# Optimization experiments

Measured on AMD Instinct MI355X. Metric: run time of the kernel, lower is better.

## Reference

```python
import jax, jax.numpy as jnp
import numpy as np
import math

N_EMBED = 1024
N_HEAD = 16
BLOCK_SIZE = 2048

def setup_inputs() -> dict:
    key = jax.random.key(0)
    k1, k2, k3, k4, k5 = jax.random.split(key, 5)
    s = 0.02
    x = jax.random.normal(k1, (2, 2048, N_EMBED), dtype=jnp.float32)
    W_qkv = jax.random.normal(k2, (N_EMBED, 3 * N_EMBED), dtype=jnp.float32) * s
    b_qkv = jax.random.normal(k3, (3 * N_EMBED,), dtype=jnp.float32) * s
    W_out = jax.random.normal(k4, (N_EMBED, N_EMBED), dtype=jnp.float32) * s
    b_out = jax.random.normal(k5, (N_EMBED,), dtype=jnp.float32) * s
    return {"x": x, "W_qkv": W_qkv, "b_qkv": b_qkv, "W_out": W_out, "b_out": b_out}

def reference(x, W_qkv, b_qkv, W_out, b_out):
    b, s, d = x.shape
    hd = d // N_HEAD  # head dim
    qkv = x @ W_qkv + b_qkv                       # [b, s, 3d]
    q, k, v = jnp.split(qkv, 3, axis=-1)
    # [b, h, s, hd]
    q = q.reshape(b, s, N_HEAD, hd).transpose(0, 2, 1, 3)
    k = k.reshape(b, s, N_HEAD, hd).transpose(0, 2, 1, 3)
    v = v.reshape(b, s, N_HEAD, hd).transpose(0, 2, 1, 3)
    scale = 1.0 / math.sqrt(hd)
    sims = jnp.einsum('bhqd,bhkd->bhqk', q, k) * scale  # [b, h, s, s]
    causal = jnp.tril(jnp.ones((s, s), dtype=bool))
    sims = jnp.where(causal[None, None], sims, -jnp.inf)
    probs = jax.nn.softmax(sims, axis=-1)
    attn = jnp.einsum('bhqk,bhkd->bhqd', probs, v)       # [b, h, s, hd]
    attn = attn.transpose(0, 2, 1, 3).reshape(b, s, d)
    return attn @ W_out + b_out
```

## Files before the change

### kernel.cpp

```cpp
#include <hip/hip_runtime.h>
#include <hip/hip_bf16.h>

typedef __attribute__((ext_vector_type(8))) short short8;
typedef __attribute__((ext_vector_type(4))) short short4v;
typedef __attribute__((ext_vector_type(4))) float f32x4;
typedef __attribute__((ext_vector_type(16))) float f32x16;
typedef __attribute__((ext_vector_type(4))) unsigned int u32x4;
typedef unsigned short u16;

__device__ __forceinline__ u16 f2bf(float f) {
  __hip_bfloat16 h = __float2bfloat16(f);
  return __builtin_bit_cast(unsigned short, h);
}

__device__ __forceinline__ unsigned pack2(float lo, float hi) {
  return (unsigned)f2bf(lo) | ((unsigned)f2bf(hi) << 16);
}

__device__ __forceinline__ void gload16(const u16* g, u16* l) {
  __builtin_amdgcn_global_load_lds(
      (const __attribute__((address_space(1))) unsigned int*)g,
      (__attribute__((address_space(3))) unsigned int*)l, 16, 0, 0);
}

__global__ void cvt_x_kernel(const float* __restrict__ in, u16* __restrict__ out, int n) {
  int i = (blockIdx.x * blockDim.x + threadIdx.x) * 4;
  if (i >= n) return;
  float4 f = *(const float4*)(in + i);
  uint2 pk;
  pk.x = pack2(f.x, f.y);
  pk.y = pack2(f.z, f.w);
  *(uint2*)(out + i) = pk;
}

__global__ void tcvt_kernel(const float* __restrict__ in, u16* __restrict__ out, int N) {
  __shared__ float tile[32][33];
  int n0 = blockIdx.x * 32, k0 = blockIdx.y * 32;
  int tx = threadIdx.x, ty = threadIdx.y;
#pragma unroll
  for (int r = 0; r < 4; ++r) {
    int k = ty + r * 8;
    tile[k][tx] = in[(size_t)(k0 + k) * N + n0 + tx];
  }
  __syncthreads();
#pragma unroll
  for (int r = 0; r < 4; ++r) {
    int n = ty + r * 8;
    out[(size_t)(n0 + n) * 1024 + k0 + tx] = f2bf(tile[tx][n]);
  }
}

template <int EPI>
__global__ __launch_bounds__(256, 2) void gemm_kernel(const u16* __restrict__ A,
                                                      const u16* __restrict__ Bt,
                                                      const float* __restrict__ bias,
                                                      void* __restrict__ outp) {
  __shared__ u16 Al[128 * 64];
  __shared__ u16 Bl[128 * 64];
  const int tid = threadIdx.x;
  const int lane = tid & 63, wid = tid >> 6;
  const int l15 = lane & 15, lg = lane >> 4;
  const int wm = wid >> 1, wn = wid & 1;
  const int m0 = blockIdx.y * 128, n0 = blockIdx.x * 128;

  f32x4 acc[4][4] = {};

  for (int k0 = 0; k0 < 1024; k0 += 64) {
    __syncthreads();
#pragma unroll
    for (int i = 0; i < 4; ++i) {
      int p = i * 4096 + tid * 16;
      int row = p >> 7;
      int lslot = ((p >> 4) & 7) ^ (row & 7);
      gload16(A + (size_t)(m0 + row) * 1024 + k0 + lslot * 8, Al + i * 2048 + wid * 512);
      gload16(Bt + (size_t)(n0 + row) * 1024 + k0 + lslot * 8, Bl + i * 2048 + wid * 512);
    }
    __syncthreads();
#pragma unroll
    for (int ks = 0; ks < 2; ++ks) {
      short8 af[4], bfr[4];
#pragma unroll
      for (int m = 0; m < 4; ++m) {
        int row = wm * 64 + m * 16 + l15;
        af[m] = *(const short8*)((const char*)Al + row * 128 + (((ks * 4 + lg) ^ (row & 7)) << 4));
      }
#pragma unroll
      for (int n = 0; n < 4; ++n) {
        int row = wn * 64 + n * 16 + l15;
        bfr[n] = *(const short8*)((const char*)Bl + row * 128 + (((ks * 4 + lg) ^ (row & 7)) << 4));
      }
#pragma unroll
      for (int m = 0; m < 4; ++m)
#pragma unroll
        for (int n = 0; n < 4; ++n)
          acc[m][n] = __builtin_amdgcn_mfma_f32_16x16x32_bf16(af[m], bfr[n], acc[m][n], 0, 0, 0);
    }
  }

  if (EPI == 0) {
    u16* qkv = (u16*)outp;
#pragma unroll
    for (int m = 0; m < 4; ++m)
#pragma unroll
      for (int n = 0; n < 4; ++n) {
        const int gcol = n0 + wn * 64 + n * 16 + l15;
        const int which = gcol >> 10, dd = gcol & 1023;
        const int h = dd >> 6, hd = dd & 63;
        const float bb = bias[gcol];
        const int grow0 = m0 + wm * 64 + m * 16 + lg * 4;
        const int b = grow0 >> 11, s0 = grow0 & 2047;
        if (which == 2) {
          const int bsub = (s0 >> 2) & 3;
          const int bper = (bsub == 1) ? 2 : (bsub == 2) ? 1 : bsub;
          const int s0p = (s0 & ~15) | (bper << 2);
          short4v pk;
#pragma unroll
          for (int j = 0; j < 4; ++j) pk[j] = (short)f2bf(acc[m][n][j] + bb);
          *(short4v*)(qkv + (size_t)2 * 4194304 + ((size_t)(b * 16 + h) * 64 + hd) * 2048 + s0p) = pk;
        } else {
          const float sc = (which == 0) ? 0.18033688011112042f : 1.0f;
#pragma unroll
          for (int j = 0; j < 4; ++j) {
            float v = (acc[m][n][j] + bb) * sc;
            qkv[(size_t)which * 4194304 + ((size_t)(b * 16 + h) * 2048 + s0 + j) * 64 + hd] = f2bf(v);
          }
        }
      }
  } else {
    float* O = (float*)outp;
#pragma unroll
    for (int m = 0; m < 4; ++m)
#pragma unroll
      for (int n = 0; n < 4; ++n) {
        const int gcol = n0 + wn * 64 + n * 16 + l15;
        const float bb = bias[gcol];
#pragma unroll
        for (int j = 0; j < 4; ++j) {
          const int grow = m0 + wm * 64 + m * 16 + lg * 4 + j;
          O[(size_t)grow * 1024 + gcol] = acc[m][n][j] + bb;
        }
      }
  }
}

__global__ __launch_bounds__(256, 2) void attn_kernel(const u16* __restrict__ Q,
                                                      const u16* __restrict__ K,
                                                      const u16* __restrict__ VT,
                                                      u16* __restrict__ Aout) {
  const int bh = blockIdx.y;
  const int p = blockIdx.x;
  const int tid = threadIdx.x, lane = tid & 63, wid = tid >> 6;
  const int l31 = lane & 31, h = lane >> 5;
  const int qs = wid & 1, kp = wid >> 1;

  __shared__ __align__(16) char smem[36864];
  u16(*Kl)[4096] = (u16(*)[4096])smem;
  u16(*Vl)[4096] = (u16(*)[4096])(smem + 16384);

  const u16* Qb = Q + (size_t)bh * 2048 * 64;
  const u16* Kb = K + (size_t)bh * 2048 * 64;
  const u16* Vb = VT + (size_t)bh * 64 * 2048;

  const int qA = p * 64 + qs * 32;
  const int qB = (31 - p) * 64 + qs * 32;
  const int R = 32 - p;

  short8 qfA[4], qfB[4];
#pragma unroll
  for (int ks = 0; ks < 4; ++ks) {
    qfA[ks] = *(const short8*)(Qb + (size_t)(qA + l31) * 64 + ks * 16 + h * 8);
    qfB[ks] = *(const short8*)(Qb + (size_t)(qB + l31) * 64 + ks * 16 + h * 8);
  }

  f32x16 accA[2] = {}, accB[2] = {};
  float mA = -1e30f, mB = -1e30f, lA = 0.f, lB = 0.f;

  auto stage = [&](int buf, size_t kb) {
#pragma unroll
    for (int i = 0; i < 2; ++i) {
      const int row = i * 32 + (tid >> 3);
      const int sc = ((tid & 7) ^ (row & 7)) * 8;
      gload16(Kb + (kb + row) * 64 + sc, &Kl[buf][i * 2048 + wid * 512]);
      gload16(Vb + (size_t)row * 2048 + kb + sc, &Vl[buf][i * 2048 + wid * 512]);
    }
  };

  stage(0, 0);
  __syncthreads();

  for (int t = 0; t < R; ++t) {
    const int cur = t & 1;
    if (t + 1 < R) stage(cur ^ 1, (size_t)(t + 1) * 64);

    const int kvbase = t * 64 + kp * 32;
    const bool actB = kvbase <= qB + 31;
    const bool actA = kvbase <= qA + 31;
    if (actB) {
      short8 kf[4], vf[2][2];
      const int krow = kp * 32 + l31;
#pragma unroll
      for (int ks = 0; ks < 4; ++ks)
        kf[ks] = *(const short8*)((const char*)&Kl[cur][0] + krow * 128 +
                                  (((ks * 2 + h) ^ (krow & 7)) << 4));
#pragma unroll
      for (int n = 0; n < 2; ++n)
#pragma unroll
        for (int ks = 0; ks < 2; ++ks) {
          const int row = n * 32 + l31;
          vf[n][ks] = *(const short8*)((const char*)&Vl[cur][0] + row * 128 +
                                       (((kp * 4 + ks * 2 + h) ^ (row & 7)) << 4));
        }

      f32x16 saB = {}, saA = {};
      __builtin_amdgcn_s_setprio(1);
#pragma unroll
      for (int ks = 0; ks < 4; ++ks)
        saB = __builtin_amdgcn_mfma_f32_32x32x16_bf16(kf[ks], qfB[ks], saB, 0, 0, 0);
      if (actA) {
#pragma unroll
        for (int ks = 0; ks < 4; ++ks)
          saA = __builtin_amdgcn_mfma_f32_32x32x16_bf16(kf[ks], qfA[ks], saA, 0, 0, 0);
      }
      __builtin_amdgcn_s_setprio(0);

      auto finish = [&](f32x16& sa, f32x16(&acc)[2], float& m, float& l, int q0) {
        if (kvbase == q0) {
#pragma unroll
          for (int r = 0; r < 16; ++r) {
            const int kvr = (r & 3) + 8 * (r >> 2) + 4 * h;
            if (kvr > l31) sa[r] = -1e30f;
          }
        }
        const float t0 = fmaxf(fmaxf(sa[0], sa[1]), sa[2]);
        const float t1 = fmaxf(fmaxf(sa[3], sa[4]), sa[5]);
        const float t2 = fmaxf(fmaxf(sa[6], sa[7]), sa[8]);
        const float t3 = fmaxf(fmaxf(sa[9], sa[10]), sa[11]);
        const float t4 = fmaxf(fmaxf(sa[12], sa[13]), sa[14]);
        float rm = fmaxf(fmaxf(fmaxf(t0, t1), t2), fmaxf(fmaxf(t3, t4), sa[15]));
        rm = fmaxf(rm, __shfl_xor(rm, 32));
        if (!__all(rm <= m + 5.0f)) {
          const float mn = fmaxf(m, rm);
          const float corr = exp2f(m - mn);
          m = mn;
          l *= corr;
#pragma unroll
          for (int n = 0; n < 2; ++n)
#pragma unroll
            for (int r = 0; r < 16; ++r) acc[n][r] *= corr;
        }
#pragma unroll
        for (int r = 0; r < 16; ++r) sa[r] = exp2f(sa[r] - m);
        float rs = (((sa[0] + sa[1]) + (sa[2] + sa[3])) + ((sa[4] + sa[5]) + (sa[6] + sa[7]))) +
                   (((sa[8] + sa[9]) + (sa[10] + sa[11])) + ((sa[12] + sa[13]) + (sa[14] + sa[15])));
        l += rs + __shfl_xor(rs, 32);
        unsigned c[8];
#pragma unroll
        for (int i = 0; i < 8; ++i) c[i] = pack2(sa[2 * i], sa[2 * i + 1]);
        const short8 pk0 = __builtin_bit_cast(short8, (u32x4){c[0], c[1], c[2], c[3]});
        const short8 pk1 = __builtin_bit_cast(short8, (u32x4){c[4], c[5], c[6], c[7]});
        __builtin_amdgcn_s_setprio(1);
#pragma unroll
        for (int n = 0; n < 2; ++n) {
          acc[n] = __builtin_amdgcn_mfma_f32_32x32x16_bf16(vf[n][0], pk0, acc[n], 0, 0, 0);
          acc[n] = __builtin_amdgcn_mfma_f32_32x32x16_bf16(vf[n][1], pk1, acc[n], 0, 0, 0);
        }
        __builtin_amdgcn_s_setprio(0);
      };

      finish(saB, accB, mB, lB, qB);
      if (actA) finish(saA, accA, mA, lA, qA);
    }
    __syncthreads();
  }

  float* comb = (float*)smem;
  float* pA = comb + ((qs * 2 + 0) * 64 + lane) * 36;
  float* pB = comb + ((qs * 2 + 1) * 64 + lane) * 36;
  if (kp == 1) {
    pA[0] = mA; pA[1] = lA;
    pB[0] = mB; pB[1] = lB;
#pragma unroll
    for (int n = 0; n < 2; ++n)
#pragma unroll
      for (int r = 0; r < 16; ++r) {
        pA[2 + n * 16 + r] = accA[n][r];
        pB[2 + n * 16 + r] = accB[n][r];
      }
  }
  __syncthreads();
  if (kp == 0) {
    const int b = bh >> 4, hh = bh & 15;
    auto merge_store = [&](const float* pp, const f32x16(&acc)[2], float m0, float l0, int q0) {
      const float m1 = pp[0], l1 = pp[1];
      const float mn = fmaxf(m0, m1);
      const float c0 = exp2f(m0 - mn), c1 = exp2f(m1 - mn);
      const float inv = 1.0f / (l0 * c0 + l1 * c1);
      u16* rowp = Aout + (size_t)(b * 2048 + q0 + l31) * 1024 + hh * 64;
#pragma unroll
      for (int n = 0; n < 2; ++n)
#pragma unroll
        for (int r = 0; r < 16; r += 2) {
          const int hd = n * 32 + (r & 3) + 8 * (r >> 2) + 4 * h;
          const float v0 = (acc[n][r] * c0 + pp[2 + n * 16 + r] * c1) * inv;
          const float v1 = (acc[n][r + 1] * c0 + pp[2 + n * 16 + r + 1] * c1) * inv;
          *(unsigned*)(rowp + hd) = pack2(v0, v1);
        }
    };
    merge_store(pA, accA, mA, lA, qA);
    merge_store(pB, accB, mB, lB, qB);
  }
}

extern "C" void kernel_launch(void* const* d_in, const int* in_sizes, int n_in,
                              void* d_out, int out_size, void* d_ws, size_t ws_size,
                              hipStream_t stream) {
  const float* x = (const float*)d_in[0];
  const float* Wqkv = (const float*)d_in[1];
  const float* bqkv = (const float*)d_in[2];
  const float* Wout = (const float*)d_in[3];
  const float* bout = (const float*)d_in[4];

  char* ws = (char*)d_ws;
  u16* Xb = (u16*)(ws + 0);
  u16* WqkvT = (u16*)(ws + 8388608);
  u16* WoutT = (u16*)(ws + 14680064);
  u16* QKV = (u16*)(ws + 16777216);
  u16* Attn = Xb;

  cvt_x_kernel<<<4096, 256, 0, stream>>>(x, Xb, 4194304);
  tcvt_kernel<<<dim3(96, 32), dim3(32, 8), 0, stream>>>(Wqkv, WqkvT, 3072);
  tcvt_kernel<<<dim3(32, 32), dim3(32, 8), 0, stream>>>(Wout, WoutT, 1024);
  gemm_kernel<0><<<dim3(24, 32), 256, 0, stream>>>(Xb, WqkvT, bqkv, QKV);
  attn_kernel<<<dim3(16, 32), 256, 0, stream>>>(QKV, QKV + 4194304, QKV + 8388608, Attn);
  gemm_kernel<1><<<dim3(8, 32), 256, 0, stream>>>(Attn, WoutT, bout, d_out);
}
```

Before: 110.4 us.

## Replace paired causal q-tile blocks with one q-tile per block, heaviest first

The attention kernel previously paired a light and a heavy query tile in each block (p and 31-p) so every block did balanced work over 16x32 blocks. Now each block handles a single 64-row query tile, launching 32x32 blocks ordered from the longest KV range to the shortest so the scheduler can backfill short tiles. This doubles the number of blocks and reduces register pressure (one set of Q fragments and accumulators), which may raise occupancy. In exchange, K/V tiles are no longer shared across two query tiles, so K/V loads from global memory roughly double per unit of work, and there are more block launches.

```diff
diff --git a/kernel.cpp b/kernel.cpp
--- a/kernel.cpp
+++ b/kernel.cpp
@@ -148,7 +148,7 @@
                                                       const u16* __restrict__ VT,
                                                       u16* __restrict__ Aout) {
   const int bh = blockIdx.y;
-  const int p = blockIdx.x;
+  const int t = 31 - blockIdx.x;
   const int tid = threadIdx.x, lane = tid & 63, wid = tid >> 6;
   const int l31 = lane & 31, h = lane >> 5;
   const int qs = wid & 1, kp = wid >> 1;
@@ -161,19 +161,16 @@
   const u16* Kb = K + (size_t)bh * 2048 * 64;
   const u16* Vb = VT + (size_t)bh * 64 * 2048;
 
-  const int qA = p * 64 + qs * 32;
-  const int qB = (31 - p) * 64 + qs * 32;
-  const int R = 32 - p;
-
-  short8 qfA[4], qfB[4];
-#pragma unroll
-  for (int ks = 0; ks < 4; ++ks) {
-    qfA[ks] = *(const short8*)(Qb + (size_t)(qA + l31) * 64 + ks * 16 + h * 8);
-    qfB[ks] = *(const short8*)(Qb + (size_t)(qB + l31) * 64 + ks * 16 + h * 8);
-  }
-
-  f32x16 accA[2] = {}, accB[2] = {};
-  float mA = -1e30f, mB = -1e30f, lA = 0.f, lB = 0.f;
+  const int q0 = t * 64 + qs * 32;
+  const int R = t + 1;
+
+  short8 qf[4];
+#pragma unroll
+  for (int ks = 0; ks < 4; ++ks)
+    qf[ks] = *(const short8*)(Qb + (size_t)(q0 + l31) * 64 + ks * 16 + h * 8);
+
+  f32x16 acc[2] = {};
+  float m = -1e30f, l = 0.f;
 
   auto stage = [&](int buf, size_t kb) {
 #pragma unroll
@@ -188,14 +185,12 @@
   stage(0, 0);
   __syncthreads();
 
-  for (int t = 0; t < R; ++t) {
-    const int cur = t & 1;
-    if (t + 1 < R) stage(cur ^ 1, (size_t)(t + 1) * 64);
-
-    const int kvbase = t * 64 + kp * 32;
-    const bool actB = kvbase <= qB + 31;
-    const bool actA = kvbase <= qA + 31;
-    if (actB) {
+  for (int tt = 0; tt < R; ++tt) {
+    const int cur = tt & 1;
+    if (tt + 1 < R) stage(cur ^ 1, (size_t)(tt + 1) * 64);
+
+    const int kvbase = tt * 64 + kp * 32;
+    if (kvbase <= q0 + 31) {
       short8 kf[4], vf[2][2];
       const int krow = kp * 32 + l31;
 #pragma unroll
@@ -211,103 +206,84 @@
                                        (((kp * 4 + ks * 2 + h) ^ (row & 7)) << 4));
         }
 
-      f32x16 saB = {}, saA = {};
+      f32x16 sa = {};
       __builtin_amdgcn_s_setprio(1);
 #pragma unroll
       for (int ks = 0; ks < 4; ++ks)
-        saB = __builtin_amdgcn_mfma_f32_32x32x16_bf16(kf[ks], qfB[ks], saB, 0, 0, 0);
-      if (actA) {
-#pragma unroll
-        for (int ks = 0; ks < 4; ++ks)
-          saA = __builtin_amdgcn_mfma_f32_32x32x16_bf16(kf[ks], qfA[ks], saA, 0, 0, 0);
-      }
+        sa = __builtin_amdgcn_mfma_f32_32x32x16_bf16(kf[ks], qf[ks], sa, 0, 0, 0);
       __builtin_amdgcn_s_setprio(0);
 
-      auto finish = [&](f32x16& sa, f32x16(&acc)[2], float& m, float& l, int q0) {
-        if (kvbase == q0) {
-#pragma unroll
-          for (int r = 0; r < 16; ++r) {
-            const int kvr = (r & 3) + 8 * (r >> 2) + 4 * h;
-            if (kvr > l31) sa[r] = -1e30f;
-          }
+      if (kvbase == q0) {
+#pragma unroll
+        for (int r = 0; r < 16; ++r) {
+          const int kvr = (r & 3) + 8 * (r >> 2) + 4 * h;
+          if (kvr > l31) sa[r] = -1e30f;
         }
-        const float t0 = fmaxf(fmaxf(sa[0], sa[1]), sa[2]);
-        const float t1 = fmaxf(fmaxf(sa[3], sa[4]), sa[5]);
-        const float t2 = fmaxf(fmaxf(sa[6], sa[7]), sa[8]);
-        const float t3 = fmaxf(fmaxf(sa[9], sa[10]), sa[11]);
-        const float t4 = fmaxf(fmaxf(sa[12], sa[13]), sa[14]);
-        float rm = fmaxf(fmaxf(fmaxf(t0, t1), t2), fmaxf(fmaxf(t3, t4), sa[15]));
-        rm = fmaxf(rm, __shfl_xor(rm, 32));
-        if (!__all(rm <= m + 5.0f)) {
-          const float mn = fmaxf(m, rm);
-          const float corr = exp2f(m - mn);
-          m = mn;
-          l *= corr;
-#pragma unroll
-          for (int n = 0; n < 2; ++n)
-#pragma unroll
-            for (int r = 0; r < 16; ++r) acc[n][r] *= corr;
-        }
-#pragma unroll
-        for (int r = 0; r < 16; ++r) sa[r] = exp2f(sa[r] - m);
-        float rs = (((sa[0] + sa[1]) + (sa[2] + sa[3])) + ((sa[4] + sa[5]) + (sa[6] + sa[7]))) +
-                   (((sa[8] + sa[9]) + (sa[10] + sa[11])) + ((sa[12] + sa[13]) + (sa[14] + sa[15])));
-        l += rs + __shfl_xor(rs, 32);
-        unsigned c[8];
-#pragma unroll
-        for (int i = 0; i < 8; ++i) c[i] = pack2(sa[2 * i], sa[2 * i + 1]);
-        const short8 pk0 = __builtin_bit_cast(short8, (u32x4){c[0], c[1], c[2], c[3]});
-        const short8 pk1 = __builtin_bit_cast(short8, (u32x4){c[4], c[5], c[6], c[7]});
-        __builtin_amdgcn_s_setprio(1);
-#pragma unroll
-        for (int n = 0; n < 2; ++n) {
-          acc[n] = __builtin_amdgcn_mfma_f32_32x32x16_bf16(vf[n][0], pk0, acc[n], 0, 0, 0);
-          acc[n] = __builtin_amdgcn_mfma_f32_32x32x16_bf16(vf[n][1], pk1, acc[n], 0, 0, 0);
-        }
-        __builtin_amdgcn_s_setprio(0);
-      };
-
-      finish(saB, accB, mB, lB, qB);
-      if (actA) finish(saA, accA, mA, lA, qA);
+      }
+      const float t0 = fmaxf(fmaxf(sa[0], sa[1]), sa[2]);
+      const float t1 = fmaxf(fmaxf(sa[3], sa[4]), sa[5]);
+      const float t2 = fmaxf(fmaxf(sa[6], sa[7]), sa[8]);
+      const float t3 = fmaxf(fmaxf(sa[9], sa[10]), sa[11]);
+      const float t4 = fmaxf(fmaxf(sa[12], sa[13]), sa[14]);
+      float rm = fmaxf(fmaxf(fmaxf(t0, t1), t2), fmaxf(fmaxf(t3, t4), sa[15]));
+      rm = fmaxf(rm, __shfl_xor(rm, 32));
+      if (!__all(rm <= m + 5.0f)) {
+        const float mn = fmaxf(m, rm);
+        const float corr = exp2f(m - mn);
+        m = mn;
+        l *= corr;
+#pragma unroll
+        for (int n = 0; n < 2; ++n)
+#pragma unroll
+          for (int r = 0; r < 16; ++r) acc[n][r] *= corr;
+      }
+#pragma unroll
+      for (int r = 0; r < 16; ++r) sa[r] = exp2f(sa[r] - m);
+      float rs = (((sa[0] + sa[1]) + (sa[2] + sa[3])) + ((sa[4] + sa[5]) + (sa[6] + sa[7]))) +
+                 (((sa[8] + sa[9]) + (sa[10] + sa[11])) + ((sa[12] + sa[13]) + (sa[14] + sa[15])));
+      l += rs + __shfl_xor(rs, 32);
+      unsigned c[8];
+#pragma unroll
+      for (int i = 0; i < 8; ++i) c[i] = pack2(sa[2 * i], sa[2 * i + 1]);
+      const short8 pk0 = __builtin_bit_cast(short8, (u32x4){c[0], c[1], c[2], c[3]});
+      const short8 pk1 = __builtin_bit_cast(short8, (u32x4){c[4], c[5], c[6], c[7]});
+      __builtin_amdgcn_s_setprio(1);
+#pragma unroll
+      for (int n = 0; n < 2; ++n) {
+        acc[n] = __builtin_amdgcn_mfma_f32_32x32x16_bf16(vf[n][0], pk0, acc[n], 0, 0, 0);
+        acc[n] = __builtin_amdgcn_mfma_f32_32x32x16_bf16(vf[n][1], pk1, acc[n], 0, 0, 0);
+      }
+      __builtin_amdgcn_s_setprio(0);
     }
     __syncthreads();
   }
 
   float* comb = (float*)smem;
-  float* pA = comb + ((qs * 2 + 0) * 64 + lane) * 36;
-  float* pB = comb + ((qs * 2 + 1) * 64 + lane) * 36;
+  float* pp = comb + (qs * 64 + lane) * 36;
   if (kp == 1) {
-    pA[0] = mA; pA[1] = lA;
-    pB[0] = mB; pB[1] = lB;
+    pp[0] = m; pp[1] = l;
 #pragma unroll
     for (int n = 0; n < 2; ++n)
 #pragma unroll
-      for (int r = 0; r < 16; ++r) {
-        pA[2 + n * 16 + r] = accA[n][r];
-        pB[2 + n * 16 + r] = accB[n][r];
-      }
+      for (int r = 0; r < 16; ++r) pp[2 + n * 16 + r] = acc[n][r];
   }
   __syncthreads();
   if (kp == 0) {
     const int b = bh >> 4, hh = bh & 15;
-    auto merge_store = [&](const float* pp, const f32x16(&acc)[2], float m0, float l0, int q0) {
-      const float m1 = pp[0], l1 = pp[1];
-      const float mn = fmaxf(m0, m1);
-      const float c0 = exp2f(m0 - mn), c1 = exp2f(m1 - mn);
-      const float inv = 1.0f / (l0 * c0 + l1 * c1);
-      u16* rowp = Aout + (size_t)(b * 2048 + q0 + l31) * 1024 + hh * 64;
-#pragma unroll
-      for (int n = 0; n < 2; ++n)
-#pragma unroll
-        for (int r = 0; r < 16; r += 2) {
-          const int hd = n * 32 + (r & 3) + 8 * (r >> 2) + 4 * h;
-          const float v0 = (acc[n][r] * c0 + pp[2 + n * 16 + r] * c1) * inv;
-          const float v1 = (acc[n][r + 1] * c0 + pp[2 + n * 16 + r + 1] * c1) * inv;
-          *(unsigned*)(rowp + hd) = pack2(v0, v1);
-        }
-    };
-    merge_store(pA, accA, mA, lA, qA);
-    merge_store(pB, accB, mB, lB, qB);
+    const float m1 = pp[0], l1 = pp[1];
+    const float mn = fmaxf(m, m1);
+    const float c0 = exp2f(m - mn), c1 = exp2f(m1 - mn);
+    const float inv = 1.0f / (l * c0 + l1 * c1);
+    u16* rowp = Aout + (size_t)(b * 2048 + q0 + l31) * 1024 + hh * 64;
+#pragma unroll
+    for (int n = 0; n < 2; ++n)
+#pragma unroll
+      for (int r = 0; r < 16; r += 2) {
+        const int hd = n * 32 + (r & 3) + 8 * (r >> 2) + 4 * h;
+        const float v0 = (acc[n][r] * c0 + pp[2 + n * 16 + r] * c1) * inv;
+        const float v1 = (acc[n][r + 1] * c0 + pp[2 + n * 16 + r + 1] * c1) * inv;
+        *(unsigned*)(rowp + hd) = pack2(v0, v1);
+      }
   }
 }
 
@@ -331,6 +307,6 @@
   tcvt_kernel<<<dim3(96, 32), dim3(32, 8), 0, stream>>>(Wqkv, WqkvT, 3072);
   tcvt_kernel<<<dim3(32, 32), dim3(32, 8), 0, stream>>>(Wout, WoutT, 1024);
   gemm_kernel<0><<<dim3(24, 32), 256, 0, stream>>>(Xb, WqkvT, bqkv, QKV);
-  attn_kernel<<<dim3(16, 32), 256, 0, stream>>>(QKV, QKV + 4194304, QKV + 8388608, Attn);
+  attn_kernel<<<dim3(32, 32), 256, 0, stream>>>(QKV, QKV + 4194304, QKV + 8388608, Attn);
   gemm_kernel<1><<<dim3(8, 32), 256, 0, stream>>>(Attn, WoutT, bout, d_out);
 }
```

Result: slower. 131.8 us (+19.4%).

## Merge conversion kernels into one launch and halve output-GEMM tile width

Applied to the files above, without the earlier changes.

Replaces the three preprocessing launches (x cast plus two weight transpose-casts) with a single prep kernel that dispatches work by block index. The output-projection GEMM is templated on tile width and now uses a 64-column N tile, doubling its grid from 256 to 512 blocks so it covers more of the GPU's compute units. This cuts launch overhead and raises occupancy for the small GEMM, at the cost of less B-tile reuse per block.

```diff
diff --git a/kernel.cpp b/kernel.cpp
--- a/kernel.cpp
+++ b/kernel.cpp
@@ -23,76 +23,100 @@
       (__attribute__((address_space(3))) unsigned int*)l, 16, 0, 0);
 }
 
-__global__ void cvt_x_kernel(const float* __restrict__ in, u16* __restrict__ out, int n) {
-  int i = (blockIdx.x * blockDim.x + threadIdx.x) * 4;
-  if (i >= n) return;
-  float4 f = *(const float4*)(in + i);
-  uint2 pk;
-  pk.x = pack2(f.x, f.y);
-  pk.y = pack2(f.z, f.w);
-  *(uint2*)(out + i) = pk;
-}
-
-__global__ void tcvt_kernel(const float* __restrict__ in, u16* __restrict__ out, int N) {
+__global__ void prep_kernel(const float* __restrict__ x,
+                            const float* __restrict__ Wqkv,
+                            const float* __restrict__ Wout,
+                            u16* __restrict__ Xb,
+                            u16* __restrict__ WqkvT,
+                            u16* __restrict__ WoutT) {
   __shared__ float tile[32][33];
-  int n0 = blockIdx.x * 32, k0 = blockIdx.y * 32;
-  int tx = threadIdx.x, ty = threadIdx.y;
+  const int b = blockIdx.x, tid = threadIdx.x;
+  if (b < 4096) {
+    const int i = (b * 256 + tid) * 4;
+    float4 f = *(const float4*)(x + i);
+    uint2 pk;
+    pk.x = pack2(f.x, f.y);
+    pk.y = pack2(f.z, f.w);
+    *(uint2*)(Xb + i) = pk;
+    return;
+  }
+  const float* in;
+  u16* out;
+  int N, bx, by;
+  if (b < 7168) {
+    in = Wqkv; out = WqkvT; N = 3072;
+    const int bb = b - 4096;
+    bx = bb % 96; by = bb / 96;
+  } else {
+    in = Wout; out = WoutT; N = 1024;
+    const int bb = b - 7168;
+    bx = bb % 32; by = bb / 32;
+  }
+  const int n0 = bx * 32, k0 = by * 32;
+  const int tx = tid & 31, ty = tid >> 5;
 #pragma unroll
   for (int r = 0; r < 4; ++r) {
-    int k = ty + r * 8;
+    const int k = ty + r * 8;
     tile[k][tx] = in[(size_t)(k0 + k) * N + n0 + tx];
   }
   __syncthreads();
 #pragma unroll
   for (int r = 0; r < 4; ++r) {
-    int n = ty + r * 8;
+    const int n = ty + r * 8;
     out[(size_t)(n0 + n) * 1024 + k0 + tx] = f2bf(tile[tx][n]);
   }
 }
 
-template <int EPI>
+template <int EPI, int BN>
 __global__ __launch_bounds__(256, 2) void gemm_kernel(const u16* __restrict__ A,
                                                       const u16* __restrict__ Bt,
                                                       const float* __restrict__ bias,
                                                       void* __restrict__ outp) {
   __shared__ u16 Al[128 * 64];
-  __shared__ u16 Bl[128 * 64];
+  __shared__ u16 Bl[BN * 64];
+  constexpr int NF = BN / 32;
   const int tid = threadIdx.x;
   const int lane = tid & 63, wid = tid >> 6;
   const int l15 = lane & 15, lg = lane >> 4;
   const int wm = wid >> 1, wn = wid & 1;
-  const int m0 = blockIdx.y * 128, n0 = blockIdx.x * 128;
-
-  f32x4 acc[4][4] = {};
+  const int m0 = blockIdx.y * 128, n0 = blockIdx.x * BN;
+
+  f32x4 acc[4][NF] = {};
 
   for (int k0 = 0; k0 < 1024; k0 += 64) {
     __syncthreads();
 #pragma unroll
     for (int i = 0; i < 4; ++i) {
-      int p = i * 4096 + tid * 16;
-      int row = p >> 7;
-      int lslot = ((p >> 4) & 7) ^ (row & 7);
+      const int p = i * 4096 + tid * 16;
+      const int row = p >> 7;
+      const int lslot = ((p >> 4) & 7) ^ (row & 7);
       gload16(A + (size_t)(m0 + row) * 1024 + k0 + lslot * 8, Al + i * 2048 + wid * 512);
+    }
+#pragma unroll
+    for (int i = 0; i < NF; ++i) {
+      const int p = i * 4096 + tid * 16;
+      const int row = p >> 7;
+      const int lslot = ((p >> 4) & 7) ^ (row & 7);
       gload16(Bt + (size_t)(n0 + row) * 1024 + k0 + lslot * 8, Bl + i * 2048 + wid * 512);
     }
     __syncthreads();
 #pragma unroll
     for (int ks = 0; ks < 2; ++ks) {
-      short8 af[4], bfr[4];
+      short8 af[4], bfr[NF];
 #pragma unroll
       for (int m = 0; m < 4; ++m) {
-        int row = wm * 64 + m * 16 + l15;
+        const int row = wm * 64 + m * 16 + l15;
         af[m] = *(const short8*)((const char*)Al + row * 128 + (((ks * 4 + lg) ^ (row & 7)) << 4));
       }
 #pragma unroll
-      for (int n = 0; n < 4; ++n) {
-        int row = wn * 64 + n * 16 + l15;
+      for (int n = 0; n < NF; ++n) {
+        const int row = wn * (BN / 2) + n * 16 + l15;
         bfr[n] = *(const short8*)((const char*)Bl + row * 128 + (((ks * 4 + lg) ^ (row & 7)) << 4));
       }
 #pragma unroll
       for (int m = 0; m < 4; ++m)
 #pragma unroll
-        for (int n = 0; n < 4; ++n)
+        for (int n = 0; n < NF; ++n)
           acc[m][n] = __builtin_amdgcn_mfma_f32_16x16x32_bf16(af[m], bfr[n], acc[m][n], 0, 0, 0);
     }
   }
@@ -102,8 +126,8 @@
 #pragma unroll
     for (int m = 0; m < 4; ++m)
 #pragma unroll
-      for (int n = 0; n < 4; ++n) {
-        const int gcol = n0 + wn * 64 + n * 16 + l15;
+      for (int n = 0; n < NF; ++n) {
+        const int gcol = n0 + wn * (BN / 2) + n * 16 + l15;
         const int which = gcol >> 10, dd = gcol & 1023;
         const int h = dd >> 6, hd = dd & 63;
         const float bb = bias[gcol];
@@ -131,8 +155,8 @@
 #pragma unroll
     for (int m = 0; m < 4; ++m)
 #pragma unroll
-      for (int n = 0; n < 4; ++n) {
-        const int gcol = n0 + wn * 64 + n * 16 + l15;
+      for (int n = 0; n < NF; ++n) {
+        const int gcol = n0 + wn * (BN / 2) + n * 16 + l15;
         const float bb = bias[gcol];
 #pragma unroll
         for (int j = 0; j < 4; ++j) {
@@ -327,10 +351,8 @@
   u16* QKV = (u16*)(ws + 16777216);
   u16* Attn = Xb;
 
-  cvt_x_kernel<<<4096, 256, 0, stream>>>(x, Xb, 4194304);
-  tcvt_kernel<<<dim3(96, 32), dim3(32, 8), 0, stream>>>(Wqkv, WqkvT, 3072);
-  tcvt_kernel<<<dim3(32, 32), dim3(32, 8), 0, stream>>>(Wout, WoutT, 1024);
-  gemm_kernel<0><<<dim3(24, 32), 256, 0, stream>>>(Xb, WqkvT, bqkv, QKV);
+  prep_kernel<<<8192, 256, 0, stream>>>(x, Wqkv, Wout, Xb, WqkvT, WoutT);
+  gemm_kernel<0, 128><<<dim3(24, 32), 256, 0, stream>>>(Xb, WqkvT, bqkv, QKV);
   attn_kernel<<<dim3(16, 32), 256, 0, stream>>>(QKV, QKV + 4194304, QKV + 8388608, Attn);
-  gemm_kernel<1><<<dim3(8, 32), 256, 0, stream>>>(Attn, WoutT, bout, d_out);
-}
+  gemm_kernel<1, 64><<<dim3(16, 32), 256, 0, stream>>>(Attn, WoutT, bout, d_out);
+}
```

Result: faster. 102.0 us (-7.6%).
